# Kernel optimization log

Hardware: AMD Instinct MI355X
Metric: run time of the kernel (lower is better)

The kernel has to match this reference:

```python
import jax, jax.numpy as jnp
import numpy as np

B, C, N = 8, 128, 4096
C2 = C // 2
BN_EPS = 1e-5


def setup_inputs() -> dict:
    key = jax.random.key(0)
    ks = jax.random.split(key, 8)
    s = 1.0 / np.sqrt(C)
    s2 = 1.0 / np.sqrt(C2)
    return {
        "x": jax.random.normal(ks[0], (B, C, N), dtype=jnp.float32),
        "w_qk": jax.random.uniform(ks[1], (C2, C), jnp.float32, -s, s),  # shared q/k weight
        "w_v": jax.random.uniform(ks[2], (C2, C), jnp.float32, -s, s),
        "b_v": jax.random.uniform(ks[3], (C2,), jnp.float32, -s, s),
        "w_x": jax.random.uniform(ks[4], (C2, C), jnp.float32, -s, s),
        "w_t": jax.random.uniform(ks[5], (C2, C2), jnp.float32, -s2, s2),
        "b_t": jax.random.uniform(ks[6], (C2,), jnp.float32, -s2, s2),
        "gamma": jnp.ones((C2,), jnp.float32),
        "beta": jnp.zeros((C2,), jnp.float32),
    }


def reference(x, w_qk, w_v, b_v, w_x, w_t, b_t, gamma, beta):
    # 1x1 convs are per-point linear maps: [B,C,N] -> [B,C2,N]
    x_q = jnp.einsum("oc,bcn->bno", w_qk, x)          # [B, N, C2]
    x_k = jnp.einsum("oc,bcn->bon", w_qk, x)          # [B, C2, N]
    x_v = jnp.einsum("oc,bcn->bon", w_v, x) + b_v[None, :, None]

    energy = jnp.einsum("bno,bom->bnm", x_q, x_k)     # [B, N, N]
    attn = jax.nn.softmax(energy, axis=-1)            # row softmax
    attn = attn / (1e-9 + attn.sum(axis=1, keepdims=True))  # column L1 renorm

    x_r = jnp.einsum("bon,bnm->bom", x_v, attn)       # [B, C2, N]
    x_c = jnp.einsum("oc,bcn->bon", w_x, x)           # [B, C2, N]

    d = x_c - x_r
    t = jnp.einsum("oi,bin->bon", w_t, d) + b_t[None, :, None]
    # BatchNorm1d (training-mode batch stats) over (B, N) per channel
    mean = t.mean(axis=(0, 2), keepdims=True)
    var = t.var(axis=(0, 2), keepdims=True)
    t_hat = (t - mean) * jax.lax.rsqrt(var + BN_EPS)
    x_r2 = jax.nn.relu(gamma[None, :, None] * t_hat + beta[None, :, None])
    return x_c + x_r2
```

## Files before the change

### kernel.cpp

```cpp
#include <hip/hip_runtime.h>

#define B_   8
#define C_   128
#define N_   4096
#define C2_  64

typedef __bf16 bf16x8 __attribute__((ext_vector_type(8)));
typedef float  f32x4  __attribute__((ext_vector_type(4)));

#define MFMA16(a, b, c) __builtin_amdgcn_mfma_f32_16x16x32_bf16((a), (b), (c), 0, 0, 0)

#define QK_SCALE 1.2011224087864498f

static __device__ __forceinline__ unsigned short f2bf(float f) {
    union { __bf16 b; unsigned short u; } cv;
    cv.b = (__bf16)f;
    return cv.u;
}
static __device__ __forceinline__ float bf2f(unsigned short u) {
    union { unsigned int u; float f; } cv;
    cv.u = ((unsigned int)u) << 16;
    return cv.f;
}

struct us4 { unsigned short a, b, c, d; };

static __device__ __forceinline__ void gl_lds16(const unsigned short* g, void* l) {
    __builtin_amdgcn_global_load_lds(
        (const __attribute__((address_space(1))) unsigned int*)g,
        (__attribute__((address_space(3))) unsigned int*)l,
        16, 0, 0);
}

__global__ __launch_bounds__(256) void k0_wcvt(
    const float* __restrict__ wq, const float* __restrict__ wv,
    const float* __restrict__ wx, unsigned short* __restrict__ wst)
{
    const int i4 = (blockIdx.x * 256 + threadIdx.x) * 4;
    const int mat = i4 >> 13;
    const float* src = (mat == 0) ? wq : (mat == 1) ? wv : wx;
    const float sc = (mat == 0) ? QK_SCALE : 1.0f;
    const float4 v = *(const float4*)(src + (i4 & 8191));
    us4 pk;
    pk.a = f2bf(v.x * sc); pk.b = f2bf(v.y * sc);
    pk.c = f2bf(v.z * sc); pk.d = f2bf(v.w * sc);
    *(us4*)(wst + i4) = pk;
}

__global__ __launch_bounds__(256) void k1_proj(
    const float* __restrict__ x, const unsigned short* __restrict__ wst,
    const float* __restrict__ b_v,
    unsigned short* __restrict__ qk_t, unsigned short* __restrict__ xv_bf,
    float* __restrict__ xc)
{
    __shared__ __align__(16) unsigned short w_lds[192 * 128];
    __shared__ __align__(16) unsigned short x_t[64 * 136];
    const int tid = threadIdx.x;
    const int wave = tid >> 6, lane = tid & 63;
    const int quad = lane >> 4, col = lane & 15;
    const int b = blockIdx.y;
    const int n0 = blockIdx.x * 64;

    #pragma unroll
    for (int it = 0; it < 12; ++it) {
        const int idx = it * 256 + tid;
        const int row = idx >> 4, seg = idx & 15;
        gl_lds16(wst + (size_t)row * 128 + (size_t)(seg ^ (row & 7)) * 8,
                 w_lds + idx * 8);
    }
    const float* xb = x + (size_t)b * C_ * N_ + n0;
    #pragma unroll
    for (int it = 0; it < 8; ++it) {
        const int idx = it * 256 + tid;
        const int c = idx >> 4, n = (idx & 15) * 4;
        const float4 v = *(const float4*)(xb + (size_t)c * N_ + n);
        x_t[(n + 0) * 136 + c] = f2bf(v.x);
        x_t[(n + 1) * 136 + c] = f2bf(v.y);
        x_t[(n + 2) * 136 + c] = f2bf(v.z);
        x_t[(n + 3) * 136 + c] = f2bf(v.w);
    }
    __syncthreads();

    const int nw = wave * 16;
    bf16x8 bfr[4];
    #pragma unroll
    for (int kt = 0; kt < 4; ++kt)
        bfr[kt] = *(const bf16x8*)&x_t[(nw + col) * 136 + kt * 32 + quad * 8];

    const int n_g = n0 + nw + col;

    #pragma unroll
    for (int ot = 0; ot < 12; ++ot) {
        f32x4 acc = {0.f, 0.f, 0.f, 0.f};
        #pragma unroll
        for (int kt = 0; kt < 4; ++kt) {
            const bf16x8 afr = *(const bf16x8*)&w_lds[
                ((ot * 16 + col) << 7) + (((kt * 4 + quad) ^ (col & 7)) << 3)];
            acc = MFMA16(afr, bfr[kt], acc);
        }
        if (ot < 4) {
            us4 pk;
            pk.a = f2bf(acc[0]); pk.b = f2bf(acc[1]);
            pk.c = f2bf(acc[2]); pk.d = f2bf(acc[3]);
            *(us4*)&qk_t[(size_t)(b * N_ + n_g) * C2_ + ot * 16 + quad * 4] = pk;
        } else if (ot < 8) {
            const float4 bv4 = *(const float4*)(b_v + (ot - 4) * 16 + quad * 4);
            const float* bvp = (const float*)&bv4;
            #pragma unroll
            for (int r = 0; r < 4; ++r)
                xv_bf[(size_t)(b * C2_ + (ot - 4) * 16 + quad * 4 + r) * N_ + n_g]
                    = f2bf(acc[r] + bvp[r]);
        } else {
            #pragma unroll
            for (int r = 0; r < 4; ++r)
                xc[(size_t)(b * C2_ + (ot - 8) * 16 + quad * 4 + r) * N_ + n_g] = acc[r];
        }
    }
}

__global__ __launch_bounds__(256) void k2_rowstats(
    const unsigned short* __restrict__ qk_t, float* __restrict__ part_rs)
{
    __shared__ __align__(16) unsigned char lds_raw[2 * 16384];
    const int tid = threadIdx.x;
    const int wave = tid >> 6, lane = tid & 63;
    const int quad = lane >> 4, col = lane & 15;
    const int b = blockIdx.x & 7;
    const int nblk = (blockIdx.x >> 3) & 31;
    const int mq = blockIdx.x >> 8;
    const int n_base = nblk * 128 + wave * 32;
    const int m_start = mq * 512;
    const unsigned short* qb = qk_t + (size_t)b * N_ * C2_;

    bf16x8 a0[2], a1[2];
    #pragma unroll
    for (int s = 0; s < 2; ++s) {
        const unsigned short* p = qb + (size_t)(n_base + s * 16 + col) * C2_ + quad * 8;
        a0[s] = *(const bf16x8*)p;
        a1[s] = *(const bf16x8*)(p + 32);
    }

    auto stage = [&](int m0, int p) {
        unsigned char* base = lds_raw + p * 16384;
        #pragma unroll
        for (int r = 0; r < 4; ++r) {
            const int idx = r * 256 + tid;
            const int row = idx >> 3, seg = idx & 7;
            gl_lds16(qb + (size_t)(m0 + row) * C2_ + (size_t)(seg ^ (row & 7)) * 8,
                     base + idx * 16);
        }
    };

    float run_s[2][4];
    #pragma unroll
    for (int s = 0; s < 2; ++s)
        #pragma unroll
        for (int r = 0; r < 4; ++r) run_s[s][r] = 0.f;

    stage(m_start, 0);

    for (int c = 0; c < 4; ++c) {
        const int p = c & 1;
        asm volatile("s_waitcnt vmcnt(0)" ::: "memory");
        __builtin_amdgcn_s_barrier();
        asm volatile("" ::: "memory");
        if (c + 1 < 4) stage(m_start + (c + 1) * 128, 1 - p);
        const unsigned short* qt = (const unsigned short*)(lds_raw + p * 16384);
        #pragma unroll
        for (int ms = 0; ms < 8; ++ms) {
            const int row = ms * 16 + col;
            const bf16x8 b0 = *(const bf16x8*)(qt + row * 64 + ((quad ^ (col & 7)) * 8));
            const bf16x8 b1 = *(const bf16x8*)(qt + row * 64 + (((4 + quad) ^ (col & 7)) * 8));
            #pragma unroll
            for (int s = 0; s < 2; ++s) {
                f32x4 acc = {0.f, 0.f, 0.f, 0.f};
                __builtin_amdgcn_s_setprio(1);
                acc = MFMA16(a0[s], b0, acc);
                acc = MFMA16(a1[s], b1, acc);
                __builtin_amdgcn_s_setprio(0);
                #pragma unroll
                for (int r = 0; r < 4; ++r)
                    run_s[s][r] += __builtin_amdgcn_exp2f(acc[r]);
            }
        }
    }

    #pragma unroll
    for (int s = 0; s < 2; ++s)
        #pragma unroll
        for (int r = 0; r < 4; ++r) {
            #pragma unroll
            for (int off = 1; off < 16; off <<= 1)
                run_s[s][r] += __shfl_xor(run_s[s][r], off, 64);
        }
    if (col == 0) {
        #pragma unroll
        for (int s = 0; s < 2; ++s)
            #pragma unroll
            for (int r = 0; r < 4; ++r)
                part_rs[((size_t)(mq * 8 + b) << 12) + n_base + s * 16 + quad * 4 + r]
                    = run_s[s][r];
    }
}

__global__ __launch_bounds__(64) void k2w(
    const float* __restrict__ part_rs, float* __restrict__ winv)
{
    const int b = blockIdx.x & 7;
    const int n = (blockIdx.x >> 3) * 64 + threadIdx.x;
    float s = 0.f;
    #pragma unroll
    for (int q = 0; q < 8; ++q)
        s += part_rs[((size_t)(q * 8 + b) << 12) + n];
    winv[b * N_ + n] = 1.0f / s;
}

__global__ __launch_bounds__(512, 4) void k3_pv(
    const unsigned short* __restrict__ qk_t, const unsigned short* __restrict__ xv_bf,
    const float* __restrict__ winv,
    unsigned short* __restrict__ yb0, unsigned short* __restrict__ yb1,
    float* __restrict__ cspart)
{
    __shared__ __align__(16) unsigned char lds_raw[32768 + 8 * 2560];
    const int tid = threadIdx.x;
    const int wave = tid >> 6, lane = tid & 63;
    const int quad = lane >> 4, col = lane & 15;
    const int nh2 = wave & 1, mh = wave >> 1;
    const int b = blockIdx.x & 7;
    const int m_blk = ((blockIdx.x >> 3) & 31) * 128;
    const int sk = blockIdx.x >> 8;
    const int n_start = sk * 2048;
    const int n_chunks = 32;
    const int m_wave = m_blk + mh * 32;
    const unsigned short* qb = qk_t + (size_t)b * N_ * C2_;
    const unsigned short* vb = xv_bf + (size_t)b * C2_ * N_;
    const float* wn = winv + b * N_;
    unsigned short* yp = (sk == 0) ? yb0 : yb1;

    bf16x8 kb0[2], kb1[2];
    #pragma unroll
    for (int g = 0; g < 2; ++g) {
        const unsigned short* p = qb + (size_t)(m_wave + g * 16 + col) * C2_ + quad * 8;
        kb0[g] = *(const bf16x8*)p;
        kb1[g] = *(const bf16x8*)(p + 32);
    }

    bf16x8 ones;
    #pragma unroll
    for (int j = 0; j < 8; ++j) ones[j] = (__bf16)1.0f;

    unsigned short* stS = (unsigned short*)(lds_raw + 32768 + wave * 2560);

    auto stage = [&](int n0, int p) {
        unsigned char* qbase = lds_raw + p * 8192;
        unsigned char* vbase = lds_raw + 16384 + p * 8192;
        const int row = tid >> 3, seg = tid & 7;
        const int ss = seg ^ (row & 7);
        gl_lds16(qb + (size_t)(n0 + row) * C2_ + (size_t)ss * 8, qbase + tid * 16);
        gl_lds16(vb + (size_t)row * N_ + n0 + ss * 8, vbase + tid * 16);
    };

    f32x4 accY[2][4];
    #pragma unroll
    for (int g = 0; g < 2; ++g)
        #pragma unroll
        for (int os = 0; os < 4; ++os) accY[g][os] = (f32x4){0.f, 0.f, 0.f, 0.f};
    f32x4 csacc[2];
    #pragma unroll
    for (int g = 0; g < 2; ++g) csacc[g] = (f32x4){0.f, 0.f, 0.f, 0.f};

    stage(n_start, 0);
    __syncthreads();

    for (int c = 0; c < n_chunks; ++c) {
        const int n0 = n_start + c * 64;
        const int p = c & 1;
        if (c + 1 < n_chunks) stage(n0 + 64, 1 - p);

        const unsigned short* qt = (const unsigned short*)(lds_raw + p * 8192);
        const unsigned short* vt = (const unsigned short*)(lds_raw + 16384 + p * 8192);

        #pragma unroll
        for (int ns = 0; ns < 2; ++ns) {
            const int row = nh2 * 32 + ns * 16 + col;
            const bf16x8 qa0 = *(const bf16x8*)(qt + row * 64 + ((quad ^ (col & 7)) * 8));
            const bf16x8 qa1 = *(const bf16x8*)(qt + row * 64 + (((4 + quad) ^ (col & 7)) * 8));
            const float4 wv4 = *(const float4*)(wn + n0 + nh2 * 32 + ns * 16 + quad * 4);
            const float* wv = (const float*)&wv4;
            #pragma unroll
            for (int g = 0; g < 2; ++g) {
                f32x4 acc = {0.f, 0.f, 0.f, 0.f};
                acc = MFMA16(qa0, kb0[g], acc);
                acc = MFMA16(qa1, kb1[g], acc);
                union { unsigned short us[4]; uint2 u2; } pk;
                #pragma unroll
                for (int r = 0; r < 4; ++r)
                    pk.us[r] = f2bf(wv[r] * __builtin_amdgcn_exp2f(acc[r]));
                *(uint2*)&stS[(g * 16 + col) * 40 + ns * 16 + quad * 4] = pk.u2;
            }
        }

        bf16x8 sB[2];
        #pragma unroll
        for (int g = 0; g < 2; ++g)
            sB[g] = *(const bf16x8*)&stS[(g * 16 + col) * 40 + quad * 8];

        #pragma unroll
        for (int g = 0; g < 2; ++g)
            csacc[g] = MFMA16(ones, sB[g], csacc[g]);

        #pragma unroll
        for (int os = 0; os < 4; ++os) {
            const bf16x8 va = *(const bf16x8*)(vt + (os * 16 + col) * 64 +
                                               (((nh2 * 4 + quad) ^ (col & 7)) * 8));
            #pragma unroll
            for (int g = 0; g < 2; ++g)
                accY[g][os] = MFMA16(va, sB[g], accY[g][os]);
        }
        __syncthreads();
    }

    float* cmb = (float*)lds_raw;
    float* csc = (float*)(lds_raw + 32768);
    if (nh2 == 1) {
        #pragma unroll
        for (int g = 0; g < 2; ++g) {
            #pragma unroll
            for (int os = 0; os < 4; ++os)
                #pragma unroll
                for (int r = 0; r < 4; ++r)
                    cmb[((mh * 8 + g * 4 + os) * 4 + r) * 64 + lane] = accY[g][os][r];
            csc[(mh * 2 + g) * 64 + lane] = csacc[g][0];
        }
    }
    __syncthreads();
    if (nh2 == 0) {
        #pragma unroll
        for (int g = 0; g < 2; ++g) {
            const float cs = csacc[g][0] + csc[(mh * 2 + g) * 64 + lane];
            if (lane < 16)
                cspart[((size_t)sk * 8 + b) * N_ + m_wave + g * 16 + lane] = cs;
            #pragma unroll
            for (int os = 0; os < 4; ++os)
                #pragma unroll
                for (int r = 0; r < 4; ++r) {
                    const float v = accY[g][os][r] +
                        cmb[((mh * 8 + g * 4 + os) * 4 + r) * 64 + lane];
                    yp[(size_t)(b * C2_ + os * 16 + quad * 4 + r) * N_ + m_wave + g * 16 + col]
                        = f2bf(v);
                }
        }
    }
}

__global__ __launch_bounds__(256) void k4_t(
    const float* __restrict__ xc, const unsigned short* __restrict__ y0,
    const unsigned short* __restrict__ y1,
    const float* __restrict__ cspart, const float* __restrict__ w_t,
    const float* __restrict__ b_t, float* __restrict__ t_buf,
    float* __restrict__ part_bn)
{
    __shared__ __align__(16) unsigned short wlds[64 * 72];
    __shared__ __align__(16) unsigned short d_t[64 * 72];
    __shared__ float cinv[64];
    const int tid = threadIdx.x;
    const int wave = tid >> 6, lane = tid & 63;
    const int quad = lane >> 4, col = lane & 15;
    const int b = blockIdx.y;
    const int n0 = blockIdx.x * 64;
    const size_t base = (size_t)b * C2_ * N_;

    #pragma unroll
    for (int it = 0; it < 4; ++it) {
        const int idx4 = it * 256 + tid;
        const int o = idx4 >> 4, i4 = (idx4 & 15) * 4;
        const float4 v = *(const float4*)(w_t + o * 64 + i4);
        us4 pk;
        pk.a = f2bf(v.x); pk.b = f2bf(v.y); pk.c = f2bf(v.z); pk.d = f2bf(v.w);
        *(us4*)&wlds[o * 72 + i4] = pk;
    }
    if (tid < 64) {
        const int n = n0 + tid;
        const float cs = cspart[(size_t)b * N_ + n] + cspart[(size_t)(8 + b) * N_ + n];
        cinv[tid] = 1.0f / (1e-9f + cs);
    }
    __syncthreads();

    #pragma unroll
    for (int it = 0; it < 4; ++it) {
        const int idx4 = it * 256 + tid;
        const int i = idx4 >> 4, n4 = (idx4 & 15) * 4;
        const size_t g = base + (size_t)i * N_ + n0 + n4;
        const float4 c4 = *(const float4*)(xc + g);
        const us4 u0 = *(const us4*)(y0 + g);
        const us4 u1 = *(const us4*)(y1 + g);
        d_t[(n4 + 0) * 72 + i] = f2bf(c4.x - (bf2f(u0.a) + bf2f(u1.a)) * cinv[n4 + 0]);
        d_t[(n4 + 1) * 72 + i] = f2bf(c4.y - (bf2f(u0.b) + bf2f(u1.b)) * cinv[n4 + 1]);
        d_t[(n4 + 2) * 72 + i] = f2bf(c4.z - (bf2f(u0.c) + bf2f(u1.c)) * cinv[n4 + 2]);
        d_t[(n4 + 3) * 72 + i] = f2bf(c4.w - (bf2f(u0.d) + bf2f(u1.d)) * cinv[n4 + 3]);
    }
    __syncthreads();

    const int ow = wave * 16;
    bf16x8 afr[2];
    #pragma unroll
    for (int kt = 0; kt < 2; ++kt)
        afr[kt] = *(const bf16x8*)&wlds[(ow + col) * 72 + kt * 32 + quad * 8];
    const float4 bt4 = *(const float4*)(b_t + ow + quad * 4);
    const float* btp = (const float*)&bt4;

    float s[4] = {0.f, 0.f, 0.f, 0.f}, q2[4] = {0.f, 0.f, 0.f, 0.f};
    #pragma unroll
    for (int ns = 0; ns < 4; ++ns) {
        f32x4 acc = {0.f, 0.f, 0.f, 0.f};
        #pragma unroll
        for (int kt = 0; kt < 2; ++kt) {
            const bf16x8 bfr = *(const bf16x8*)&d_t[(ns * 16 + col) * 72 + kt * 32 + quad * 8];
            acc = MFMA16(afr[kt], bfr, acc);
        }
        #pragma unroll
        for (int r = 0; r < 4; ++r) {
            const float t = acc[r] + btp[r];
            t_buf[base + (size_t)(ow + quad * 4 + r) * N_ + n0 + ns * 16 + col] = t;
            s[r] += t;
            q2[r] += t * t;
        }
    }
    #pragma unroll
    for (int r = 0; r < 4; ++r) {
        #pragma unroll
        for (int off = 1; off < 16; off <<= 1) {
            s[r]  += __shfl_xor(s[r],  off, 64);
            q2[r] += __shfl_xor(q2[r], off, 64);
        }
    }
    if (col == 0) {
        const int blk = blockIdx.x * 8 + b;
        #pragma unroll
        for (int r = 0; r < 4; ++r) {
            part_bn[(size_t)(ow + quad * 4 + r) * 512 + blk]      = s[r];
            part_bn[(size_t)(64 + ow + quad * 4 + r) * 512 + blk] = q2[r];
        }
    }
}

__global__ __launch_bounds__(256) void k5r(
    const float* __restrict__ part_bn, float* __restrict__ bn)
{
    const int c = blockIdx.x;
    const int tid = threadIdx.x, wave = tid >> 6, lane = tid & 63;
    float s = 0.f;
    for (int j = tid; j < 512; j += 256) s += part_bn[(size_t)c * 512 + j];
    #pragma unroll
    for (int off = 1; off < 64; off <<= 1) s += __shfl_xor(s, off, 64);
    __shared__ float red[4];
    if (lane == 0) red[wave] = s;
    __syncthreads();
    if (tid == 0) bn[c] = red[0] + red[1] + red[2] + red[3];
}

__global__ __launch_bounds__(256) void k6_out(
    const float* __restrict__ xc, const float* __restrict__ t_buf,
    const float* __restrict__ bn, const float* __restrict__ gamma,
    const float* __restrict__ beta, float* __restrict__ out)
{
    const int idx = blockIdx.x * 256 + threadIdx.x;
    const int o = (idx >> 10) & 63;
    const float invC = 1.0f / (float)(B_ * N_);
    const float mean = bn[o] * invC;
    const float var  = bn[64 + o] * invC - mean * mean;
    const float sc = gamma[o] * rsqrtf(var + 1e-5f);
    const float sh = beta[o] - mean * sc;
    const float4 t4 = ((const float4*)t_buf)[idx];
    const float4 c4 = ((const float4*)xc)[idx];
    float4 r;
    r.x = c4.x + fmaxf(0.f, sc * t4.x + sh);
    r.y = c4.y + fmaxf(0.f, sc * t4.y + sh);
    r.z = c4.z + fmaxf(0.f, sc * t4.z + sh);
    r.w = c4.w + fmaxf(0.f, sc * t4.w + sh);
    ((float4*)out)[idx] = r;
}

extern "C" void kernel_launch(void* const* d_in, const int* in_sizes, int n_in,
                              void* d_out, int out_size, void* d_ws, size_t ws_size,
                              hipStream_t stream) {
    const float* x     = (const float*)d_in[0];
    const float* w_qk  = (const float*)d_in[1];
    const float* w_v   = (const float*)d_in[2];
    const float* b_v   = (const float*)d_in[3];
    const float* w_x   = (const float*)d_in[4];
    const float* w_t   = (const float*)d_in[5];
    const float* b_t   = (const float*)d_in[6];
    const float* gamma = (const float*)d_in[7];
    const float* beta  = (const float*)d_in[8];
    float* out = (float*)d_out;

    char* ws = (char*)d_ws;
    unsigned short* qk_t  = (unsigned short*)ws;
    unsigned short* xv_bf = (unsigned short*)(ws + (4  << 20));
    float* xc      = (float*)(ws + (8  << 20));
    unsigned short* yb0 = (unsigned short*)(ws + (16 << 20));
    unsigned short* yb1 = (unsigned short*)(ws + (20 << 20));
    float* t_buf   = (float*)(ws + (24 << 20));
    float* part_rs = (float*)(ws + (32 << 20));
    float* cspart  = (float*)(ws + (32 << 20));
    float* part_bn = (float*)(ws + (33 << 20));
    float* bn      = (float*)(ws + (33 << 20) + (256 << 10));
    unsigned short* wstack = (unsigned short*)d_out;
    float* winv = (float*)((char*)d_out + (256 << 10));

    hipLaunchKernelGGL(k0_wcvt,     dim3(24),     256, 0, stream, w_qk, w_v, w_x, wstack);
    hipLaunchKernelGGL(k1_proj,     dim3(64, 8),  256, 0, stream,
                       x, wstack, b_v, qk_t, xv_bf, xc);
    hipLaunchKernelGGL(k2_rowstats, dim3(2048),   256, 0, stream, qk_t, part_rs);
    hipLaunchKernelGGL(k2w,         dim3(512),    64,  0, stream, part_rs, winv);
    hipLaunchKernelGGL(k3_pv,       dim3(512),    512, 0, stream,
                       qk_t, xv_bf, winv, yb0, yb1, cspart);
    hipLaunchKernelGGL(k4_t,        dim3(64, 8),  256, 0, stream,
                       xc, yb0, yb1, cspart, w_t, b_t, t_buf, part_bn);
    hipLaunchKernelGGL(k5r,         dim3(128),    256, 0, stream, part_bn, bn);
    hipLaunchKernelGGL(k6_out,      dim3(2048),   256, 0, stream, xc, t_buf, bn, gamma, beta, out);
}
```

Before: 168.6 us.

## Exploit energy symmetry in row-sum pass and fold normalizer into MFMA accumulator

Because q and k share a weight, the energy matrix is symmetric. The row-sum kernel now computes only upper-triangular 128x128 tiles and emits both row and column partial sums from each, which roughly halves the exp/MFMA work. The per-row normalizer is stored as -log2(sum) and used as the MFMA accumulator's initial value, so the PV kernel no longer needs a multiply after the exp. This adds more partial-sum buffers (32 instead of 8) and a per-block triangular index loop, and it relies on the energy being symmetric.

```diff
diff --git a/kernel.cpp b/kernel.cpp
--- a/kernel.cpp
+++ b/kernel.cpp
@@ -118,20 +118,21 @@
     }
 }
 
-__global__ __launch_bounds__(256) void k2_rowstats(
+__global__ __launch_bounds__(256) void k2_sym(
     const unsigned short* __restrict__ qk_t, float* __restrict__ part_rs)
 {
-    __shared__ __align__(16) unsigned char lds_raw[2 * 16384];
+    __shared__ __align__(16) unsigned short slab[128 * 64];
+    __shared__ float cwl[4 * 128];
     const int tid = threadIdx.x;
     const int wave = tid >> 6, lane = tid & 63;
     const int quad = lane >> 4, col = lane & 15;
     const int b = blockIdx.x & 7;
-    const int nblk = (blockIdx.x >> 3) & 31;
-    const int mq = blockIdx.x >> 8;
-    const int n_base = nblk * 128 + wave * 32;
-    const int m_start = mq * 512;
+    int job = blockIdx.x >> 3, ti = 0;
+    while (job >= 32 - ti) { job -= 32 - ti; ++ti; }
+    const int tj = ti + job;
     const unsigned short* qb = qk_t + (size_t)b * N_ * C2_;
 
+    const int n_base = ti * 128 + wave * 32;
     bf16x8 a0[2], a1[2];
     #pragma unroll
     for (int s = 0; s < 2; ++s) {
@@ -140,16 +141,14 @@
         a1[s] = *(const bf16x8*)(p + 32);
     }
 
-    auto stage = [&](int m0, int p) {
-        unsigned char* base = lds_raw + p * 16384;
-        #pragma unroll
-        for (int r = 0; r < 4; ++r) {
-            const int idx = r * 256 + tid;
-            const int row = idx >> 3, seg = idx & 7;
-            gl_lds16(qb + (size_t)(m0 + row) * C2_ + (size_t)(seg ^ (row & 7)) * 8,
-                     base + idx * 16);
-        }
-    };
+    #pragma unroll
+    for (int r = 0; r < 4; ++r) {
+        const int idx = r * 256 + tid;
+        const int row = idx >> 3, seg = idx & 7;
+        gl_lds16(qb + (size_t)(tj * 128 + row) * C2_ + (size_t)(seg ^ (row & 7)) * 8,
+                 slab + idx * 8);
+    }
+    __syncthreads();
 
     float run_s[2][4];
     #pragma unroll
@@ -157,32 +156,34 @@
         #pragma unroll
         for (int r = 0; r < 4; ++r) run_s[s][r] = 0.f;
 
-    stage(m_start, 0);
-
-    for (int c = 0; c < 4; ++c) {
-        const int p = c & 1;
-        asm volatile("s_waitcnt vmcnt(0)" ::: "memory");
-        __builtin_amdgcn_s_barrier();
-        asm volatile("" ::: "memory");
-        if (c + 1 < 4) stage(m_start + (c + 1) * 128, 1 - p);
-        const unsigned short* qt = (const unsigned short*)(lds_raw + p * 16384);
-        #pragma unroll
-        for (int ms = 0; ms < 8; ++ms) {
-            const int row = ms * 16 + col;
-            const bf16x8 b0 = *(const bf16x8*)(qt + row * 64 + ((quad ^ (col & 7)) * 8));
-            const bf16x8 b1 = *(const bf16x8*)(qt + row * 64 + (((4 + quad) ^ (col & 7)) * 8));
-            #pragma unroll
-            for (int s = 0; s < 2; ++s) {
-                f32x4 acc = {0.f, 0.f, 0.f, 0.f};
-                __builtin_amdgcn_s_setprio(1);
-                acc = MFMA16(a0[s], b0, acc);
-                acc = MFMA16(a1[s], b1, acc);
-                __builtin_amdgcn_s_setprio(0);
-                #pragma unroll
-                for (int r = 0; r < 4; ++r)
-                    run_s[s][r] += __builtin_amdgcn_exp2f(acc[r]);
+    #pragma unroll
+    for (int g = 0; g < 8; ++g) {
+        const int row = g * 16 + col;
+        const bf16x8 b0 = *(const bf16x8*)(slab + row * 64 + ((quad ^ (col & 7)) * 8));
+        const bf16x8 b1 = *(const bf16x8*)(slab + row * 64 + (((4 + quad) ^ (col & 7)) * 8));
+        float cs = 0.f;
+        #pragma unroll
+        for (int s = 0; s < 2; ++s) {
+            f32x4 acc = {0.f, 0.f, 0.f, 0.f};
+            __builtin_amdgcn_s_setprio(1);
+            acc = MFMA16(a0[s], b0, acc);
+            acc = MFMA16(a1[s], b1, acc);
+            __builtin_amdgcn_s_setprio(0);
+            #pragma unroll
+            for (int r = 0; r < 4; ++r) {
+                const float u = __builtin_amdgcn_exp2f(acc[r]);
+                run_s[s][r] += u;
+                cs += u;
             }
         }
+        cs += __shfl_xor(cs, 16, 64);
+        cs += __shfl_xor(cs, 32, 64);
+        if (quad == 0) cwl[wave * 128 + g * 16 + col] = cs;
+    }
+    __syncthreads();
+    if (ti != tj && tid < 128) {
+        const float c = cwl[tid] + cwl[128 + tid] + cwl[256 + tid] + cwl[384 + tid];
+        part_rs[((size_t)(ti * 8 + b) << 12) + tj * 128 + tid] = c;
     }
 
     #pragma unroll
@@ -198,26 +199,26 @@
         for (int s = 0; s < 2; ++s)
             #pragma unroll
             for (int r = 0; r < 4; ++r)
-                part_rs[((size_t)(mq * 8 + b) << 12) + n_base + s * 16 + quad * 4 + r]
+                part_rs[((size_t)(tj * 8 + b) << 12) + n_base + s * 16 + quad * 4 + r]
                     = run_s[s][r];
     }
 }
 
 __global__ __launch_bounds__(64) void k2w(
-    const float* __restrict__ part_rs, float* __restrict__ winv)
+    const float* __restrict__ part_rs, float* __restrict__ lw)
 {
     const int b = blockIdx.x & 7;
     const int n = (blockIdx.x >> 3) * 64 + threadIdx.x;
     float s = 0.f;
     #pragma unroll
-    for (int q = 0; q < 8; ++q)
-        s += part_rs[((size_t)(q * 8 + b) << 12) + n];
-    winv[b * N_ + n] = 1.0f / s;
+    for (int t = 0; t < 32; ++t)
+        s += part_rs[((size_t)(t * 8 + b) << 12) + n];
+    lw[b * N_ + n] = -__log2f(s);
 }
 
 __global__ __launch_bounds__(512, 4) void k3_pv(
     const unsigned short* __restrict__ qk_t, const unsigned short* __restrict__ xv_bf,
-    const float* __restrict__ winv,
+    const float* __restrict__ lw,
     unsigned short* __restrict__ yb0, unsigned short* __restrict__ yb1,
     float* __restrict__ cspart)
 {
@@ -234,7 +235,7 @@
     const int m_wave = m_blk + mh * 32;
     const unsigned short* qb = qk_t + (size_t)b * N_ * C2_;
     const unsigned short* vb = xv_bf + (size_t)b * C2_ * N_;
-    const float* wn = winv + b * N_;
+    const float* ln = lw + b * N_;
     unsigned short* yp = (sk == 0) ? yb0 : yb1;
 
     bf16x8 kb0[2], kb1[2];
@@ -285,17 +286,16 @@
             const int row = nh2 * 32 + ns * 16 + col;
             const bf16x8 qa0 = *(const bf16x8*)(qt + row * 64 + ((quad ^ (col & 7)) * 8));
             const bf16x8 qa1 = *(const bf16x8*)(qt + row * 64 + (((4 + quad) ^ (col & 7)) * 8));
-            const float4 wv4 = *(const float4*)(wn + n0 + nh2 * 32 + ns * 16 + quad * 4);
-            const float* wv = (const float*)&wv4;
+            const float4 lw4 = *(const float4*)(ln + n0 + nh2 * 32 + ns * 16 + quad * 4);
             #pragma unroll
             for (int g = 0; g < 2; ++g) {
-                f32x4 acc = {0.f, 0.f, 0.f, 0.f};
+                f32x4 acc = {lw4.x, lw4.y, lw4.z, lw4.w};
                 acc = MFMA16(qa0, kb0[g], acc);
                 acc = MFMA16(qa1, kb1[g], acc);
                 union { unsigned short us[4]; uint2 u2; } pk;
                 #pragma unroll
                 for (int r = 0; r < 4; ++r)
-                    pk.us[r] = f2bf(wv[r] * __builtin_amdgcn_exp2f(acc[r]));
+                    pk.us[r] = f2bf(__builtin_amdgcn_exp2f(acc[r]));
                 *(uint2*)&stS[(g * 16 + col) * 40 + ns * 16 + quad * 4] = pk.u2;
             }
         }
@@ -502,20 +502,20 @@
     unsigned short* yb0 = (unsigned short*)(ws + (16 << 20));
     unsigned short* yb1 = (unsigned short*)(ws + (20 << 20));
     float* t_buf   = (float*)(ws + (24 << 20));
-    float* part_rs = (float*)(ws + (32 << 20));
+    float* part_rs = (float*)(ws + (16 << 20));
     float* cspart  = (float*)(ws + (32 << 20));
     float* part_bn = (float*)(ws + (33 << 20));
     float* bn      = (float*)(ws + (33 << 20) + (256 << 10));
     unsigned short* wstack = (unsigned short*)d_out;
-    float* winv = (float*)((char*)d_out + (256 << 10));
+    float* lw = (float*)((char*)d_out + (256 << 10));
 
     hipLaunchKernelGGL(k0_wcvt,     dim3(24),     256, 0, stream, w_qk, w_v, w_x, wstack);
     hipLaunchKernelGGL(k1_proj,     dim3(64, 8),  256, 0, stream,
                        x, wstack, b_v, qk_t, xv_bf, xc);
-    hipLaunchKernelGGL(k2_rowstats, dim3(2048),   256, 0, stream, qk_t, part_rs);
-    hipLaunchKernelGGL(k2w,         dim3(512),    64,  0, stream, part_rs, winv);
+    hipLaunchKernelGGL(k2_sym,      dim3(4224),   256, 0, stream, qk_t, part_rs);
+    hipLaunchKernelGGL(k2w,         dim3(512),    64,  0, stream, part_rs, lw);
     hipLaunchKernelGGL(k3_pv,       dim3(512),    512, 0, stream,
-                       qk_t, xv_bf, winv, yb0, yb1, cspart);
+                       qk_t, xv_bf, lw, yb0, yb1, cspart);
     hipLaunchKernelGGL(k4_t,        dim3(64, 8),  256, 0, stream,
                        xc, yb0, yb1, cspart, w_t, b_t, t_buf, part_bn);
     hipLaunchKernelGGL(k5r,         dim3(128),    256, 0, stream, part_bn, bn);
```

Result: no change. 167.7 us (-0.5%).
